# Kernel optimization log

Measured on AMD Instinct MI355X. Metric: run time of the kernel, lower is better.

Reference implementation:

```python
import jax, jax.numpy as jnp
import numpy as np

B, T, E = 2, 2048, 1024
H = 16
D = E // H  # head_dim = 64


def setup_inputs() -> dict:
    key = jax.random.key(0)
    k1, k2, k3 = jax.random.split(key, 3)
    x = jax.random.normal(k1, (B, T, E), dtype=jnp.float32)
    w_qkv = jax.random.normal(k2, (3 * E, E), dtype=jnp.float32) * 0.02
    w_proj = jax.random.normal(k3, (E, E), dtype=jnp.float32) * 0.02
    return {"x": x, "w_qkv": w_qkv, "w_proj": w_proj}


def reference(x, w_qkv, w_proj):
    b, t, c = x.shape
    # qkv projection (torch Linear: x @ W^T), split into q,k,v
    qkv = jnp.einsum('btc,fc->btf', x, w_qkv)  # [B,T,3E]
    q, k, v = jnp.split(qkv, 3, axis=-1)
    # [B,T,E] -> [B,H,T,D]
    q = q.reshape(b, t, H, D).transpose(0, 2, 1, 3)
    k = k.reshape(b, t, H, D).transpose(0, 2, 1, 3)
    v = v.reshape(b, t, H, D).transpose(0, 2, 1, 3)
    scale = 1.0 / jnp.sqrt(jnp.float32(D))
    att = jnp.einsum('bhqd,bhkd->bhqk', q, k) * scale  # [B,H,T,T]
    causal = jnp.tril(jnp.ones((t, t), dtype=bool))
    att = jnp.where(causal[None, None], att, -jnp.inf)
    att = jax.nn.softmax(att, axis=-1)
    out = jnp.einsum('bhqk,bhkd->bhqd', att, v)  # [B,H,T,D]
    out = out.transpose(0, 2, 1, 3).reshape(b, t, c)  # [B,T,E]
    out = jnp.einsum('btc,oc->bto', out, w_proj)
    return out
```

## Files before the change

### kernel.cpp

```cpp
#include <hip/hip_runtime.h>
#include <stdint.h>
#include <stddef.h>

typedef __attribute__((ext_vector_type(8))) short s16x8;
typedef __attribute__((ext_vector_type(4))) short s16x4;
typedef __attribute__((ext_vector_type(4))) float f32x4;

#define B_  2
#define T_  2048
#define E_  1024
#define H_  16
#define E3_ 3072

__device__ __forceinline__ short f2bf(float f) {
  union { float f; uint32_t u; } v; v.f = f;
  uint32_t u = v.u;
  return (short)((u + 0x7FFFu + ((u >> 16) & 1u)) >> 16);
}

__device__ __forceinline__ uint32_t fbits(float f) {
  union { float f; uint32_t u; } v; v.f = f; return v.u;
}

__device__ __forceinline__ void gload_lds16(const short* g, short* l) {
  __builtin_amdgcn_global_load_lds(
      (__attribute__((address_space(1))) void*)(const_cast<short*>(g)),
      (__attribute__((address_space(3))) void*)(l), 16, 0, 0);
}

__global__ void castk_all(const float* __restrict__ x, const float* __restrict__ wqkv,
                          const float* __restrict__ wproj, short* __restrict__ xb,
                          short* __restrict__ wqkvb, short* __restrict__ wprojb) {
  const int bid = blockIdx.x;
  const float* in; short* out; int i; float sc = 1.0f;
  if (bid < 4096)      { in = x;     out = xb;     i = bid * 256 + threadIdx.x; }
  else if (bid < 7168) { in = wqkv;  out = wqkvb;  i = (bid - 4096) * 256 + threadIdx.x;
                         if (i < 262144) sc = 0.18033688011112042f; }
  else                 { in = wproj; out = wprojb; i = (bid - 7168) * 256 + threadIdx.x; }
  const float4 v = ((const float4*)in)[i];
  s16x4 o;
  o[0] = f2bf(v.x * sc); o[1] = f2bf(v.y * sc);
  o[2] = f2bf(v.z * sc); o[3] = f2bf(v.w * sc);
  ((s16x4*)out)[i] = o;
}

template <int MODE>
__global__ void gemm_nt_128(const short* __restrict__ A, const short* __restrict__ B,
                            void* __restrict__ Cv, short* __restrict__ vt,
                            int M, int N, int K) {
  __shared__ short As[128 * 32];
  __shared__ short Bs[128 * 32];
  const int tid  = threadIdx.x;
  const int lane = tid & 63;
  const int w    = tid >> 6;
  const int quad = lane >> 4;
  const int l16  = lane & 15;
  const int wm   = (w >> 1) * 64;
  const int wn   = (w & 1) * 64;
  const int bm   = blockIdx.y * 128;
  const int bn   = blockIdx.x * 128;

  f32x4 acc[4][4];
#pragma unroll
  for (int i = 0; i < 4; i++)
#pragma unroll
    for (int j = 0; j < 4; j++) acc[i][j] = (f32x4){0.f, 0.f, 0.f, 0.f};

  const int srow = w * 32 + (lane >> 2);
  const int scol = (lane & 3) * 8;
  const short* gA = A + (size_t)(bm + srow) * K + scol;
  const short* gB = B + (size_t)(bn + srow) * K + scol;
  short* lA = As + (w * 32) * 32;
  short* lB = Bs + (w * 32) * 32;

  for (int k0 = 0; k0 < K; k0 += 32) {
    __syncthreads();
    gload_lds16(gA + k0,          lA);
    gload_lds16(gA + 16 * K + k0, lA + 16 * 32);
    gload_lds16(gB + k0,          lB);
    gload_lds16(gB + 16 * K + k0, lB + 16 * 32);
    __syncthreads();

    s16x8 a[4], b[4];
#pragma unroll
    for (int i = 0; i < 4; i++)
      a[i] = *(const s16x8*)&As[(wm + i * 16 + l16) * 32 + quad * 8];
#pragma unroll
    for (int j = 0; j < 4; j++)
      b[j] = *(const s16x8*)&Bs[(wn + j * 16 + l16) * 32 + quad * 8];
#pragma unroll
    for (int i = 0; i < 4; i++)
#pragma unroll
      for (int j = 0; j < 4; j++)
        acc[i][j] = __builtin_amdgcn_mfma_f32_16x16x32_bf16(a[i], b[j], acc[i][j], 0, 0, 0);
  }

  if (MODE == 2 && bn >= 2 * E_) {
#pragma unroll
    for (int i = 0; i < 4; i++) {
      const int token = bm + wm + i * 16 + quad * 4;
      const int bb = token >> 11, t = token & (T_ - 1);
#pragma unroll
      for (int j = 0; j < 4; j++) {
        const int col = bn + wn + j * 16 + l16 - 2 * E_;
        s16x4 pk;
#pragma unroll
        for (int r = 0; r < 4; r++) pk[r] = f2bf(acc[i][j][r]);
        *(s16x4*)&vt[((size_t)(bb * H_ + (col >> 6)) * 64 + (col & 63)) * T_ + t] = pk;
      }
    }
  } else {
#pragma unroll
    for (int i = 0; i < 4; i++) {
      const int row0 = bm + wm + i * 16 + quad * 4;
#pragma unroll
      for (int j = 0; j < 4; j++) {
        const int col = bn + wn + j * 16 + l16;
#pragma unroll
        for (int r = 0; r < 4; r++) {
          const size_t idx = (size_t)(row0 + r) * N + col;
          if (MODE == 2) ((short*)Cv)[idx] = f2bf(acc[i][j][r]);
          else           ((float*)Cv)[idx] = acc[i][j][r];
        }
      }
    }
  }
}

__global__ void __launch_bounds__(256, 2)
attn_kernel(const short* __restrict__ qkv, const short* __restrict__ vt,
            short* __restrict__ attout) {
  __shared__ short Ks[2][64 * 64];
  __shared__ short Vs[2][64 * 64];
  __shared__ short Ps[4][16 * 64];
  const int tid  = threadIdx.x;
  const int lane = tid & 63;
  const int w    = tid >> 6;
  const int quad = lane >> 4;
  const int l16  = lane & 15;
  const int bh = blockIdx.x;
  const int b = bh >> 4, h = bh & 15;
  const int pr = blockIdx.y;
  const float NEG_INF = -__builtin_inff();

  const int srl = lane >> 3;
  const int sgc = ((lane & 7) ^ srl) * 8;
  const short* gK = qkv + (size_t)(b * T_) * E3_ + E_ + h * 64 + sgc;
  const short* gV = vt + (size_t)(bh * 64) * T_ + sgc;
  const int swz = (l16 & 7);

  s16x8 ones;
#pragma unroll
  for (int i = 0; i < 8; i++) ones[i] = (short)0x3F80;

  auto stage = [&](int kv0s, int bf) {
#pragma unroll
    for (int i = 0; i < 2; i++) {
      const int row = w * 16 + i * 8 + srl;
      gload_lds16(gK + (size_t)(kv0s + row) * E3_, &Ks[bf][(w * 16 + i * 8) * 64]);
      gload_lds16(gV + (size_t)row * T_ + kv0s,    &Vs[bf][(w * 16 + i * 8) * 64]);
    }
  };

  stage(0, 0);
  __syncthreads();

  int g = 0;
#pragma unroll 1
  for (int ph = 0; ph < 2; ph++) {
    const int qt  = ph ? (31 - pr) : pr;
    const int q0b = qt * 64;
    const int q0w = q0b + w * 16;

    const short* qbase = qkv + (size_t)(b * T_ + q0w + l16) * E3_ + h * 64 + quad * 8;
    const s16x8 qf0 = *(const s16x8*)(qbase);
    const s16x8 qf1 = *(const s16x8*)(qbase + 32);

    f32x4 o[4]; f32x4 ol = (f32x4){0.f, 0.f, 0.f, 0.f};
#pragma unroll
    for (int j = 0; j < 4; j++) o[j] = (f32x4){0.f, 0.f, 0.f, 0.f};

    for (int kv0 = 0; kv0 <= q0b; kv0 += 64, g++) {
      const int cur = g & 1;

      s16x8 kf[2][4];
#pragma unroll
      for (int c = 0; c < 2; c++)
#pragma unroll
        for (int j = 0; j < 4; j++)
          kf[c][j] = *(const s16x8*)&Ks[cur][(j * 16 + l16) * 64 + (((c * 4 + quad) ^ swz) * 8)];

      if (kv0 + 64 <= q0b) stage(kv0 + 64, cur ^ 1);
      else if (ph == 0)    stage(0, cur ^ 1);

      f32x4 s[4];
#pragma unroll
      for (int j = 0; j < 4; j++) s[j] = (f32x4){0.f, 0.f, 0.f, 0.f};
#pragma unroll
      for (int c = 0; c < 2; c++)
#pragma unroll
        for (int j = 0; j < 4; j++)
          s[j] = __builtin_amdgcn_mfma_f32_16x16x32_bf16(kf[c][j], c == 0 ? qf0 : qf1, s[j], 0, 0, 0);

      if (kv0 == q0b) {
#pragma unroll
        for (int j = 0; j < 4; j++)
#pragma unroll
          for (int r = 0; r < 4; r++)
            if (j * 16 + quad * 4 + r > w * 16 + l16) s[j][r] = NEG_INF;
      }

#pragma unroll
      for (int j = 0; j < 4; j++) {
        const float p0 = exp2f(s[j][0]);
        const float p1 = exp2f(s[j][1]);
        const float p2 = exp2f(s[j][2]);
        const float p3 = exp2f(s[j][3]);
        int2 pk;
        pk.x = (int)__builtin_amdgcn_perm(fbits(p1), fbits(p0), 0x07060302u);
        pk.y = (int)__builtin_amdgcn_perm(fbits(p3), fbits(p2), 0x07060302u);
        short* pw = &Ps[w][l16 * 64 + (((2 * j + (quad >> 1)) ^ swz) * 8) + (quad & 1) * 4];
        *(int2*)pw = pk;
      }
      __asm volatile("s_waitcnt lgkmcnt(0)" ::: "memory");

#pragma unroll
      for (int c = 0; c < 2; c++) {
        const s16x8 pf = *(const s16x8*)&Ps[w][l16 * 64 + (((4 * c + quad) ^ swz) * 8)];
        ol = __builtin_amdgcn_mfma_f32_16x16x32_bf16(pf, ones, ol, 0, 0, 0);
#pragma unroll
        for (int j = 0; j < 4; j++) {
          const s16x8 vf = *(const s16x8*)&Vs[cur][(j * 16 + l16) * 64 + (((c * 4 + quad) ^ swz) * 8)];
          o[j] = __builtin_amdgcn_mfma_f32_16x16x32_bf16(pf, vf, o[j], 0, 0, 0);
        }
      }

      __syncthreads();
    }

#pragma unroll
    for (int r = 0; r < 4; r++) {
      const float inv = 1.0f / ol[r];
      const int q = q0w + quad * 4 + r;
      short* ob = attout + ((size_t)(b * T_ + q) * H_ + h) * 64 + l16;
      ob[0]  = f2bf(o[0][r] * inv);
      ob[16] = f2bf(o[1][r] * inv);
      ob[32] = f2bf(o[2][r] * inv);
      ob[48] = f2bf(o[3][r] * inv);
    }
  }
}

extern "C" void kernel_launch(void* const* d_in, const int* in_sizes, int n_in,
                              void* d_out, int out_size, void* d_ws, size_t ws_size,
                              hipStream_t stream) {
  const float* x     = (const float*)d_in[0];
  const float* wqkv  = (const float*)d_in[1];
  const float* wproj = (const float*)d_in[2];

  if (ws_size < 58720256u) return;
  short* ws     = (short*)d_ws;
  short* xb     = ws;
  short* wqkvb  = xb + 4194304;
  short* wprojb = wqkvb + 3145728;
  short* qkv    = wprojb + 1048576;
  short* vt     = qkv + 12582912;
  short* attb   = vt + 4194304;

  castk_all<<<8192, 256, 0, stream>>>(x, wqkv, wproj, xb, wqkvb, wprojb);
  gemm_nt_128<2><<<dim3(24, 32), 256, 0, stream>>>(xb, wqkvb, qkv, vt, 4096, 3072, 1024);
  attn_kernel<<<dim3(32, 16), 256, 0, stream>>>(qkv, vt, attb);
  gemm_nt_128<0><<<dim3(8, 32), 256, 0, stream>>>(attb, wprojb, d_out, nullptr, 4096, 1024, 1024);
}
```

Before: 175.8 us.

## Split paired causal query tiles into separate blocks, longest first

The attention kernel no longer pairs a short and a long causal query tile in one block. It now launches one block per query tile (grid 32x32), ordered so the longest tiles start first. Launch bounds are raised to 4 blocks per CU, and LDS offsets are precomputed into registers. This targets low occupancy and load imbalance, in exchange for more blocks, repeated K/V staging setup, and tighter register limits that could cause spills.

```diff
diff --git a/kernel.cpp b/kernel.cpp
--- a/kernel.cpp
+++ b/kernel.cpp
@@ -127,7 +127,7 @@
   }
 }
 
-__global__ void __launch_bounds__(256, 2)
+__global__ void __launch_bounds__(256, 4)
 attn_kernel(const short* __restrict__ qkv, const short* __restrict__ vt,
             short* __restrict__ attout) {
   __shared__ short Ks[2][64 * 64];
@@ -140,7 +140,9 @@
   const int l16  = lane & 15;
   const int bh = blockIdx.x;
   const int b = bh >> 4, h = bh & 15;
-  const int pr = blockIdx.y;
+  const int qt = 31 - (int)blockIdx.y;
+  const int q0b = qt * 64;
+  const int q0w = q0b + w * 16;
   const float NEG_INF = -__builtin_inff();
 
   const int srl = lane >> 3;
@@ -149,9 +151,25 @@
   const short* gV = vt + (size_t)(bh * 64) * T_ + sgc;
   const int swz = (l16 & 7);
 
+  const short* qbase = qkv + (size_t)(b * T_ + q0w + l16) * E3_ + h * 64 + quad * 8;
+  const s16x8 qf0 = *(const s16x8*)(qbase);
+  const s16x8 qf1 = *(const s16x8*)(qbase + 32);
+
   s16x8 ones;
 #pragma unroll
   for (int i = 0; i < 8; i++) ones[i] = (short)0x3F80;
+
+  int koff[2][4], pfoff[2], pwoff[4];
+#pragma unroll
+  for (int c = 0; c < 2; c++) {
+#pragma unroll
+    for (int j = 0; j < 4; j++)
+      koff[c][j] = 2 * ((j * 16 + l16) * 64 + (((c * 4 + quad) ^ swz) * 8));
+    pfoff[c] = 2 * (l16 * 64 + (((4 * c + quad) ^ swz) * 8));
+  }
+#pragma unroll
+  for (int j = 0; j < 4; j++)
+    pwoff[j] = 2 * (l16 * 64 + (((2 * j + (quad >> 1)) ^ swz) * 8) + (quad & 1) * 4);
 
   auto stage = [&](int kv0s, int bf) {
 #pragma unroll
@@ -162,92 +180,82 @@
     }
   };
 
+  f32x4 o[4]; f32x4 ol = (f32x4){0.f, 0.f, 0.f, 0.f};
+#pragma unroll
+  for (int j = 0; j < 4; j++) o[j] = (f32x4){0.f, 0.f, 0.f, 0.f};
+
   stage(0, 0);
   __syncthreads();
 
-  int g = 0;
-#pragma unroll 1
-  for (int ph = 0; ph < 2; ph++) {
-    const int qt  = ph ? (31 - pr) : pr;
-    const int q0b = qt * 64;
-    const int q0w = q0b + w * 16;
-
-    const short* qbase = qkv + (size_t)(b * T_ + q0w + l16) * E3_ + h * 64 + quad * 8;
-    const s16x8 qf0 = *(const s16x8*)(qbase);
-    const s16x8 qf1 = *(const s16x8*)(qbase + 32);
-
-    f32x4 o[4]; f32x4 ol = (f32x4){0.f, 0.f, 0.f, 0.f};
-#pragma unroll
-    for (int j = 0; j < 4; j++) o[j] = (f32x4){0.f, 0.f, 0.f, 0.f};
-
-    for (int kv0 = 0; kv0 <= q0b; kv0 += 64, g++) {
-      const int cur = g & 1;
-
-      s16x8 kf[2][4];
-#pragma unroll
-      for (int c = 0; c < 2; c++)
-#pragma unroll
-        for (int j = 0; j < 4; j++)
-          kf[c][j] = *(const s16x8*)&Ks[cur][(j * 16 + l16) * 64 + (((c * 4 + quad) ^ swz) * 8)];
-
-      if (kv0 + 64 <= q0b) stage(kv0 + 64, cur ^ 1);
-      else if (ph == 0)    stage(0, cur ^ 1);
-
-      f32x4 s[4];
-#pragma unroll
-      for (int j = 0; j < 4; j++) s[j] = (f32x4){0.f, 0.f, 0.f, 0.f};
-#pragma unroll
-      for (int c = 0; c < 2; c++)
-#pragma unroll
-        for (int j = 0; j < 4; j++)
-          s[j] = __builtin_amdgcn_mfma_f32_16x16x32_bf16(kf[c][j], c == 0 ? qf0 : qf1, s[j], 0, 0, 0);
-
-      if (kv0 == q0b) {
-#pragma unroll
-        for (int j = 0; j < 4; j++)
-#pragma unroll
-          for (int r = 0; r < 4; r++)
-            if (j * 16 + quad * 4 + r > w * 16 + l16) s[j][r] = NEG_INF;
+  for (int kv0 = 0; kv0 <= q0b; kv0 += 64) {
+    const int cur = (kv0 >> 6) & 1;
+
+    if (kv0 + 64 <= q0b) stage(kv0 + 64, cur ^ 1);
+
+    const char* kb = (const char*)&Ks[cur][0];
+    const char* vb = (const char*)&Vs[cur][0];
+    char* pb = (char*)&Ps[w][0];
+
+    s16x8 kf[2][4];
+#pragma unroll
+    for (int c = 0; c < 2; c++)
+#pragma unroll
+      for (int j = 0; j < 4; j++)
+        kf[c][j] = *(const s16x8*)(kb + koff[c][j]);
+
+    f32x4 s[4];
+#pragma unroll
+    for (int j = 0; j < 4; j++) s[j] = (f32x4){0.f, 0.f, 0.f, 0.f};
+#pragma unroll
+    for (int c = 0; c < 2; c++)
+#pragma unroll
+      for (int j = 0; j < 4; j++)
+        s[j] = __builtin_amdgcn_mfma_f32_16x16x32_bf16(kf[c][j], c == 0 ? qf0 : qf1, s[j], 0, 0, 0);
+
+    if (kv0 == q0b) {
+#pragma unroll
+      for (int j = 0; j < 4; j++)
+#pragma unroll
+        for (int r = 0; r < 4; r++)
+          if (j * 16 + quad * 4 + r > w * 16 + l16) s[j][r] = NEG_INF;
+    }
+
+#pragma unroll
+    for (int j = 0; j < 4; j++) {
+      const float p0 = exp2f(s[j][0]);
+      const float p1 = exp2f(s[j][1]);
+      const float p2 = exp2f(s[j][2]);
+      const float p3 = exp2f(s[j][3]);
+      int2 pk;
+      pk.x = (int)__builtin_amdgcn_perm(fbits(p1), fbits(p0), 0x07060302u);
+      pk.y = (int)__builtin_amdgcn_perm(fbits(p3), fbits(p2), 0x07060302u);
+      *(int2*)(pb + pwoff[j]) = pk;
+    }
+    __asm volatile("s_waitcnt lgkmcnt(0)" ::: "memory");
+
+#pragma unroll
+    for (int c = 0; c < 2; c++) {
+      const s16x8 pf = *(const s16x8*)(pb + pfoff[c]);
+      ol = __builtin_amdgcn_mfma_f32_16x16x32_bf16(pf, ones, ol, 0, 0, 0);
+#pragma unroll
+      for (int j = 0; j < 4; j++) {
+        const s16x8 vf = *(const s16x8*)(vb + koff[c][j]);
+        o[j] = __builtin_amdgcn_mfma_f32_16x16x32_bf16(pf, vf, o[j], 0, 0, 0);
       }
-
-#pragma unroll
-      for (int j = 0; j < 4; j++) {
-        const float p0 = exp2f(s[j][0]);
-        const float p1 = exp2f(s[j][1]);
-        const float p2 = exp2f(s[j][2]);
-        const float p3 = exp2f(s[j][3]);
-        int2 pk;
-        pk.x = (int)__builtin_amdgcn_perm(fbits(p1), fbits(p0), 0x07060302u);
-        pk.y = (int)__builtin_amdgcn_perm(fbits(p3), fbits(p2), 0x07060302u);
-        short* pw = &Ps[w][l16 * 64 + (((2 * j + (quad >> 1)) ^ swz) * 8) + (quad & 1) * 4];
-        *(int2*)pw = pk;
-      }
-      __asm volatile("s_waitcnt lgkmcnt(0)" ::: "memory");
-
-#pragma unroll
-      for (int c = 0; c < 2; c++) {
-        const s16x8 pf = *(const s16x8*)&Ps[w][l16 * 64 + (((4 * c + quad) ^ swz) * 8)];
-        ol = __builtin_amdgcn_mfma_f32_16x16x32_bf16(pf, ones, ol, 0, 0, 0);
-#pragma unroll
-        for (int j = 0; j < 4; j++) {
-          const s16x8 vf = *(const s16x8*)&Vs[cur][(j * 16 + l16) * 64 + (((c * 4 + quad) ^ swz) * 8)];
-          o[j] = __builtin_amdgcn_mfma_f32_16x16x32_bf16(pf, vf, o[j], 0, 0, 0);
-        }
-      }
-
-      __syncthreads();
-    }
-
-#pragma unroll
-    for (int r = 0; r < 4; r++) {
-      const float inv = 1.0f / ol[r];
-      const int q = q0w + quad * 4 + r;
-      short* ob = attout + ((size_t)(b * T_ + q) * H_ + h) * 64 + l16;
-      ob[0]  = f2bf(o[0][r] * inv);
-      ob[16] = f2bf(o[1][r] * inv);
-      ob[32] = f2bf(o[2][r] * inv);
-      ob[48] = f2bf(o[3][r] * inv);
-    }
+    }
+
+    __syncthreads();
+  }
+
+#pragma unroll
+  for (int r = 0; r < 4; r++) {
+    const float inv = 1.0f / ol[r];
+    const int q = q0w + quad * 4 + r;
+    short* ob = attout + ((size_t)(b * T_ + q) * H_ + h) * 64 + l16;
+    ob[0]  = f2bf(o[0][r] * inv);
+    ob[16] = f2bf(o[1][r] * inv);
+    ob[32] = f2bf(o[2][r] * inv);
+    ob[48] = f2bf(o[3][r] * inv);
   }
 }
 
@@ -269,6 +277,6 @@
 
   castk_all<<<8192, 256, 0, stream>>>(x, wqkv, wproj, xb, wqkvb, wprojb);
   gemm_nt_128<2><<<dim3(24, 32), 256, 0, stream>>>(xb, wqkvb, qkv, vt, 4096, 3072, 1024);
-  attn_kernel<<<dim3(32, 16), 256, 0, stream>>>(qkv, vt, attb);
+  attn_kernel<<<dim3(32, 32), 256, 0, stream>>>(qkv, vt, attb);
   gemm_nt_128<0><<<dim3(8, 32), 256, 0, stream>>>(attb, wprojb, d_out, nullptr, 4096, 1024, 1024);
 }
```

New measurement: 179.7 us. 1.02x slower.
